# Performance work log

Measured on AMD Instinct MI355X. Metric: run time of the kernel, lower is better.

## Reference

```python
import jax, jax.numpy as jnp
import numpy as np


def _nn_mean_sqdist(source, target):
    # source: [N,3], target: [M,3]
    s_norm = jnp.sum(source ** 2, axis=1, keepdims=True)          # [N,1]
    t_norm = jnp.sum(target ** 2, axis=1, keepdims=True)          # [M,1]
    dist = s_norm + t_norm.T - 2.0 * (source @ target.T)          # [N,M] squared dists
    return jnp.min(dist, axis=1).mean()


def setup_inputs() -> dict:
    key = jax.random.key(0)
    k1, k2 = jax.random.split(key)
    pred_positions = jax.random.normal(k1, (16384, 3), dtype=jnp.float32)
    target_positions = jax.random.normal(k2, (16384, 3), dtype=jnp.float32)
    return {"pred_positions": pred_positions, "target_positions": target_positions}


def reference(pred_positions, target_positions):
    d_pt = _nn_mean_sqdist(pred_positions, target_positions)
    d_tp = _nn_mean_sqdist(target_positions, pred_positions)  # use_bidirectional=True
    return (d_pt + d_tp) / 2.0
```

## Files before the change

kernel.cpp:

```cpp
#include <hip/hip_runtime.h>

#define TPB 256

typedef __attribute__((ext_vector_type(8))) short bf16x8;
typedef __attribute__((ext_vector_type(16))) float f32x16;

__device__ inline unsigned short f2bf(float f) {
    unsigned u = __float_as_uint(f);
    return (unsigned short)((u + 0x7FFFu + ((u >> 16) & 1u)) >> 16);
}
__device__ inline float bf2f(unsigned short h) {
    return __uint_as_float((unsigned)h << 16);
}
__device__ inline uint4 pack8(unsigned short s0, unsigned short s1,
                              unsigned short s2, unsigned short s3,
                              unsigned short s4, unsigned short s5,
                              unsigned short s6, unsigned short s7) {
    uint4 v;
    v.x = (unsigned)s0 | ((unsigned)s1 << 16);
    v.y = (unsigned)s2 | ((unsigned)s3 << 16);
    v.z = (unsigned)s4 | ((unsigned)s5 << 16);
    v.w = (unsigned)s6 | ((unsigned)s7 << 16);
    return v;
}
__device__ inline bf16x8 as_frag(uint4 v) {
    union { uint4 u; bf16x8 f; } c; c.u = v; return c.f;
}

__global__ __launch_bounds__(TPB) void prep_kernel(
        const float* __restrict__ a, const float* __restrict__ b,
        uint4* __restrict__ pAa, uint4* __restrict__ pBa,
        uint4* __restrict__ pAb, uint4* __restrict__ pBb,
        float* __restrict__ norms, unsigned* __restrict__ pmins,
        float* __restrict__ acc, unsigned* __restrict__ cnt, int n) {
    int idx = blockIdx.x * TPB + threadIdx.x;
    if (idx < 2 * n) {
        int isB = idx >= n;
        int i = isB ? idx - n : idx;
        const float* s = isB ? b : a;
        float x = s[3 * i], y = s[3 * i + 1], z = s[3 * i + 2];
        float w = x * x + y * y + z * z;
        norms[idx] = w;
        float ax = -2.0f * x, ay = -2.0f * y, az = -2.0f * z;
        unsigned short ahx = f2bf(ax), ahy = f2bf(ay), ahz = f2bf(az);
        unsigned short alx = f2bf(ax - bf2f(ahx));
        unsigned short aly = f2bf(ay - bf2f(ahy));
        unsigned short alz = f2bf(az - bf2f(ahz));
        unsigned short thx = f2bf(x), thy = f2bf(y), thz = f2bf(z);
        unsigned short tlx = f2bf(x - bf2f(thx));
        unsigned short tly = f2bf(y - bf2f(thy));
        unsigned short tlz = f2bf(z - bf2f(thz));
        unsigned short wh = f2bf(w);  float r1 = w - bf2f(wh);
        unsigned short wm = f2bf(r1); float r2 = r1 - bf2f(wm);
        unsigned short wl = f2bf(r2);
        const unsigned short ONE = 0x3F80;
        uint4* Ad = (isB ? pAb : pAa) + (size_t)i * 2;
        uint4* Bd = (isB ? pBb : pBa) + (size_t)i * 2;
        Ad[0] = pack8(ahx, ahy, ahz, alx, aly, alz, ahx, ahy);
        Ad[1] = pack8(ahz, ONE, ONE, ONE, alx, aly, alz, 0);
        Bd[0] = pack8(thx, thy, thz, thx, thy, thz, tlx, tly);
        Bd[1] = pack8(tlz, wh, wm, wl, tlx, tly, tlz, 0);
        pmins[idx] = 0xFFFFFFFFu;
    }
    if (idx == 0) { acc[0] = 0.0f; cnt[0] = 0u; }
}

__global__ __launch_bounds__(TPB, 4) void minpass_kernel(
        const uint4* __restrict__ pAa, const uint4* __restrict__ pBa,
        const uint4* __restrict__ pAb, const uint4* __restrict__ pBb,
        const float* __restrict__ norms, unsigned* __restrict__ pmins, int n) {
    const int TS = 8;
    const int NRB = n / 256;
    const int TGT = n / TS;
    const int NIT = TGT / 64;

    int bid = blockIdx.x;
    int dir = bid / (NRB * TS);
    int rem = bid % (NRB * TS);
    int rbk = rem / TS;
    int ts  = rem % TS;

    const uint4* __restrict__ Ap = dir ? pAb : pAa;
    const uint4* __restrict__ Bp = dir ? pBa : pBb;

    const int tid = threadIdx.x;
    const int wid = tid >> 6, lane = tid & 63;
    const int lr = lane & 31, lh = lane >> 5;

    const int rowbase = rbk * 256 + wid * 64;
    bf16x8 a0 = as_frag(Ap[(size_t)(rowbase + lr) * 2 + lh]);
    bf16x8 a1 = as_frag(Ap[(size_t)(rowbase + 32 + lr) * 2 + lh]);

    float rm0[16], rm1[16];
#pragma unroll
    for (int i = 0; i < 16; ++i) { rm0[i] = __builtin_inff(); rm1[i] = __builtin_inff(); }
    f32x16 z = {};

    const uint4* __restrict__ bp = Bp + (size_t)(ts * TGT + lr) * 2 + lh;

#define PAIR_ITER(B0, B1) do {                                                  \
    bf16x8 b0 = as_frag(B0), b1 = as_frag(B1);                                  \
    f32x16 dX = __builtin_amdgcn_mfma_f32_32x32x16_bf16(a0, b0, z, 0, 0, 0);    \
    f32x16 dY = __builtin_amdgcn_mfma_f32_32x32x16_bf16(a0, b1, z, 0, 0, 0);    \
    _Pragma("unroll")                                                           \
    for (int i = 0; i < 16; ++i)                                                \
        rm0[i] = fminf(rm0[i], fminf(dX[i], dY[i]));             \
    dX = __builtin_amdgcn_mfma_f32_32x32x16_bf16(a1, b0, z, 0, 0, 0);           \
    dY = __builtin_amdgcn_mfma_f32_32x32x16_bf16(a1, b1, z, 0, 0, 0);           \
    _Pragma("unroll")                                                           \
    for (int i = 0; i < 16; ++i)                                                \
        rm1[i] = fminf(rm1[i], fminf(dX[i], dY[i]));                            \
} while (0)

    uint4 P0 = bp[0], P1 = bp[64], P2 = bp[128], P3 = bp[192];
    for (int j = 0; j + 4 <= NIT; j += 2) {
        PAIR_ITER(P0, P1);
        P0 = bp[(size_t)(2 * j + 4) * 64];
        P1 = bp[(size_t)(2 * j + 5) * 64];
        PAIR_ITER(P2, P3);
        P2 = bp[(size_t)(2 * j + 6) * 64];
        P3 = bp[(size_t)(2 * j + 7) * 64];
    }
    PAIR_ITER(P0, P1);
    PAIR_ITER(P2, P3);

#pragma unroll
    for (int k = 1; k < 32; k <<= 1) {
#pragma unroll
        for (int i = 0; i < 16; ++i) {
            rm0[i] = fminf(rm0[i], __shfl_xor(rm0[i], k, 64));
            rm1[i] = fminf(rm1[i], __shfl_xor(rm1[i], k, 64));
        }
    }
    if (lr == 0) {
        unsigned* pm = pmins + (size_t)dir * n;
        const float* nb = norms + (dir ? n : 0);
        int rb0 = rowbase + lh * 4;
#pragma unroll
        for (int i = 0; i < 16; ++i) {
            int r = (i & 3) + ((i >> 2) << 3);
            int r0 = rb0 + r, r1 = rb0 + 32 + r;
            atomicMin(&pm[r0], __float_as_uint(rm0[i] + nb[r0]));
            atomicMin(&pm[r1], __float_as_uint(rm1[i] + nb[r1]));
        }
    }
#undef PAIR_ITER
}

__global__ __launch_bounds__(TPB) void finalize_kernel(
        const uint4* __restrict__ pmins, float* __restrict__ acc,
        unsigned* __restrict__ cnt, float* __restrict__ out, int n, int nblocks) {
    int i = blockIdx.x * TPB + threadIdx.x;
    uint4 v = pmins[i];
    float sum = __uint_as_float(v.x) + __uint_as_float(v.y)
              + __uint_as_float(v.z) + __uint_as_float(v.w);
    for (int off = 32; off > 0; off >>= 1)
        sum += __shfl_down(sum, off, 64);
    __shared__ float wsum[TPB / 64];
    int lane = threadIdx.x & 63, wid = threadIdx.x >> 6;
    if (lane == 0) wsum[wid] = sum;
    __syncthreads();
    if (threadIdx.x == 0) {
        float t = 0.0f;
        for (int w = 0; w < TPB / 64; ++w) t += wsum[w];
        atomicAdd(acc, t);
        __threadfence();
        unsigned old = atomicAdd(cnt, 1u);
        if (old == (unsigned)(nblocks - 1)) {
            float a0 = atomicAdd(acc, 0.0f);
            out[0] = a0 / (float)(2 * n);
        }
    }
}

extern "C" void kernel_launch(void* const* d_in, const int* in_sizes, int n_in,
                              void* d_out, int out_size, void* d_ws, size_t ws_size,
                              hipStream_t stream) {
    const float* a = (const float*)d_in[0];
    const float* b = (const float*)d_in[1];
    int n = in_sizes[0] / 3;
    float* out = (float*)d_out;
    char* ws = (char*)d_ws;
    float* acc = (float*)ws;
    unsigned* cnt = (unsigned*)(ws + 8);
    float* norms = (float*)(ws + 256);
    char* packs = ws + 256 + (size_t)2 * n * 4;
    size_t psz = (size_t)n * 32;
    uint4* pAa = (uint4*)(packs);
    uint4* pBa = (uint4*)(packs + psz);
    uint4* pAb = (uint4*)(packs + 2 * psz);
    uint4* pBb = (uint4*)(packs + 3 * psz);
    unsigned* pmins = (unsigned*)(packs + 4 * psz);

    prep_kernel<<<(2 * n + TPB - 1) / TPB, TPB, 0, stream>>>(
        a, b, pAa, pBa, pAb, pBb, norms, pmins, acc, cnt, n);
    int mblocks = 2 * (n / 256) * 8;
    minpass_kernel<<<mblocks, TPB, 0, stream>>>(
        pAa, pBa, pAb, pBb, norms, pmins, n);
    int fblocks = (2 * n / 4) / TPB;
    finalize_kernel<<<fblocks, TPB, 0, stream>>>(
        (const uint4*)pmins, acc, cnt, out, n, fblocks);
}
```

Before: 97.86 us.

## Fold both squared norms into the MFMA and issue four MFMAs per pair

The source-point norm is now packed into the A fragment (wh,wm,wl against ONE in B), so the MFMA output is the full squared distance. This removes the norms buffer, its writes in prep and the per-row norm loads and adds in the atomicMin epilogue. The alpha-split low terms of the dot product are dropped from the second k-half, which changes which cross terms enter the sum and may slightly reduce precision. The four MFMAs per pair are now issued back to back before a merged min loop, with the launch-bounds occupancy hint lowered from 4 to 3 to give room for the extra live accumulators.

Result: slower. 100.1 us (+2.3%).

```diff
diff --git a/kernel.cpp b/kernel.cpp
--- a/kernel.cpp
+++ b/kernel.cpp
@@ -30,17 +30,17 @@
 __global__ __launch_bounds__(TPB) void prep_kernel(
         const float* __restrict__ a, const float* __restrict__ b,
         uint4* __restrict__ pAa, uint4* __restrict__ pBa,
-        uint4* __restrict__ pAb, uint4* __restrict__ pBb,
-        float* __restrict__ norms, unsigned* __restrict__ pmins,
+        uint4* __restrict__ pAt, uint4* __restrict__ pBt,
+        unsigned* __restrict__ pmins,
         float* __restrict__ acc, unsigned* __restrict__ cnt, int n) {
     int idx = blockIdx.x * TPB + threadIdx.x;
+    const unsigned short ONE = 0x3F80;
     if (idx < 2 * n) {
-        int isB = idx >= n;
-        int i = isB ? idx - n : idx;
-        const float* s = isB ? b : a;
+        int isT = idx >= n;
+        int i = isT ? idx - n : idx;
+        const float* s = isT ? b : a;
         float x = s[3 * i], y = s[3 * i + 1], z = s[3 * i + 2];
         float w = x * x + y * y + z * z;
-        norms[idx] = w;
         float ax = -2.0f * x, ay = -2.0f * y, az = -2.0f * z;
         unsigned short ahx = f2bf(ax), ahy = f2bf(ay), ahz = f2bf(az);
         unsigned short alx = f2bf(ax - bf2f(ahx));
@@ -53,26 +53,25 @@
         unsigned short wh = f2bf(w);  float r1 = w - bf2f(wh);
         unsigned short wm = f2bf(r1); float r2 = r1 - bf2f(wm);
         unsigned short wl = f2bf(r2);
-        const unsigned short ONE = 0x3F80;
-        uint4* Ad = (isB ? pAb : pAa) + (size_t)i * 2;
-        uint4* Bd = (isB ? pBb : pBa) + (size_t)i * 2;
+        uint4* Ad = (isT ? pAt : pAa) + (size_t)i * 2;
+        uint4* Bd = (isT ? pBt : pBa) + (size_t)i * 2;
         Ad[0] = pack8(ahx, ahy, ahz, alx, aly, alz, ahx, ahy);
-        Ad[1] = pack8(ahz, ONE, ONE, ONE, alx, aly, alz, 0);
+        Ad[1] = pack8(ahz, wh, wm, wl, ONE, ONE, ONE, 0);
         Bd[0] = pack8(thx, thy, thz, thx, thy, thz, tlx, tly);
-        Bd[1] = pack8(tlz, wh, wm, wl, tlx, tly, tlz, 0);
+        Bd[1] = pack8(tlz, ONE, ONE, ONE, wh, wm, wl, 0);
         pmins[idx] = 0xFFFFFFFFu;
     }
     if (idx == 0) { acc[0] = 0.0f; cnt[0] = 0u; }
 }
 
-__global__ __launch_bounds__(TPB, 4) void minpass_kernel(
+__global__ __launch_bounds__(TPB, 3) void minpass_kernel(
         const uint4* __restrict__ pAa, const uint4* __restrict__ pBa,
-        const uint4* __restrict__ pAb, const uint4* __restrict__ pBb,
-        const float* __restrict__ norms, unsigned* __restrict__ pmins, int n) {
+        const uint4* __restrict__ pAt, const uint4* __restrict__ pBt,
+        unsigned* __restrict__ pmins, int n) {
     const int TS = 8;
     const int NRB = n / 256;
     const int TGT = n / TS;
-    const int NIT = TGT / 64;
+    const int NP = TGT / 64;
 
     int bid = blockIdx.x;
     int dir = bid / (NRB * TS);
@@ -80,8 +79,8 @@
     int rbk = rem / TS;
     int ts  = rem % TS;
 
-    const uint4* __restrict__ Ap = dir ? pAb : pAa;
-    const uint4* __restrict__ Bp = dir ? pBa : pBb;
+    const uint4* __restrict__ Ap = dir ? pAt : pAa;
+    const uint4* __restrict__ Bp = dir ? pBa : pBt;
 
     const int tid = threadIdx.x;
     const int wid = tid >> 6, lane = tid & 63;
@@ -100,29 +99,29 @@
 
 #define PAIR_ITER(B0, B1) do {                                                  \
     bf16x8 b0 = as_frag(B0), b1 = as_frag(B1);                                  \
-    f32x16 dX = __builtin_amdgcn_mfma_f32_32x32x16_bf16(a0, b0, z, 0, 0, 0);    \
-    f32x16 dY = __builtin_amdgcn_mfma_f32_32x32x16_bf16(a0, b1, z, 0, 0, 0);    \
+    f32x16 d00 = __builtin_amdgcn_mfma_f32_32x32x16_bf16(a0, b0, z, 0, 0, 0);   \
+    f32x16 d01 = __builtin_amdgcn_mfma_f32_32x32x16_bf16(a0, b1, z, 0, 0, 0);   \
+    f32x16 d10 = __builtin_amdgcn_mfma_f32_32x32x16_bf16(a1, b0, z, 0, 0, 0);   \
+    f32x16 d11 = __builtin_amdgcn_mfma_f32_32x32x16_bf16(a1, b1, z, 0, 0, 0);   \
     _Pragma("unroll")                                                           \
-    for (int i = 0; i < 16; ++i)                                                \
-        rm0[i] = fminf(rm0[i], fminf(dX[i], dY[i]));             \
-    dX = __builtin_amdgcn_mfma_f32_32x32x16_bf16(a1, b0, z, 0, 0, 0);           \
-    dY = __builtin_amdgcn_mfma_f32_32x32x16_bf16(a1, b1, z, 0, 0, 0);           \
-    _Pragma("unroll")                                                           \
-    for (int i = 0; i < 16; ++i)                                                \
-        rm1[i] = fminf(rm1[i], fminf(dX[i], dY[i]));                            \
+    for (int i = 0; i < 16; ++i) {                                              \
+        rm0[i] = fminf(rm0[i], fminf(d00[i], d01[i]));           \
+        rm1[i] = fminf(rm1[i], fminf(d10[i], d11[i]));           \
+    }                                                                           \
 } while (0)
 
     uint4 P0 = bp[0], P1 = bp[64], P2 = bp[128], P3 = bp[192];
-    for (int j = 0; j + 4 <= NIT; j += 2) {
+    for (int p = 0; p + 4 <= NP; p += 2) {
         PAIR_ITER(P0, P1);
-        P0 = bp[(size_t)(2 * j + 4) * 64];
-        P1 = bp[(size_t)(2 * j + 5) * 64];
+        P0 = bp[(size_t)(2 * p + 4) * 64];
+        P1 = bp[(size_t)(2 * p + 5) * 64];
         PAIR_ITER(P2, P3);
-        P2 = bp[(size_t)(2 * j + 6) * 64];
-        P3 = bp[(size_t)(2 * j + 7) * 64];
+        P2 = bp[(size_t)(2 * p + 6) * 64];
+        P3 = bp[(size_t)(2 * p + 7) * 64];
     }
     PAIR_ITER(P0, P1);
     PAIR_ITER(P2, P3);
+#undef PAIR_ITER
 
 #pragma unroll
     for (int k = 1; k < 32; k <<= 1) {
@@ -134,17 +133,14 @@
     }
     if (lr == 0) {
         unsigned* pm = pmins + (size_t)dir * n;
-        const float* nb = norms + (dir ? n : 0);
         int rb0 = rowbase + lh * 4;
 #pragma unroll
         for (int i = 0; i < 16; ++i) {
             int r = (i & 3) + ((i >> 2) << 3);
-            int r0 = rb0 + r, r1 = rb0 + 32 + r;
-            atomicMin(&pm[r0], __float_as_uint(rm0[i] + nb[r0]));
-            atomicMin(&pm[r1], __float_as_uint(rm1[i] + nb[r1]));
+            atomicMin(&pm[rb0 + r], __float_as_uint(rm0[i]));
+            atomicMin(&pm[rb0 + 32 + r], __float_as_uint(rm1[i]));
         }
     }
-#undef PAIR_ITER
 }
 
 __global__ __launch_bounds__(TPB) void finalize_kernel(
@@ -183,20 +179,19 @@
     char* ws = (char*)d_ws;
     float* acc = (float*)ws;
     unsigned* cnt = (unsigned*)(ws + 8);
-    float* norms = (float*)(ws + 256);
-    char* packs = ws + 256 + (size_t)2 * n * 4;
+    char* packs = ws + 256;
     size_t psz = (size_t)n * 32;
     uint4* pAa = (uint4*)(packs);
     uint4* pBa = (uint4*)(packs + psz);
-    uint4* pAb = (uint4*)(packs + 2 * psz);
-    uint4* pBb = (uint4*)(packs + 3 * psz);
+    uint4* pAt = (uint4*)(packs + 2 * psz);
+    uint4* pBt = (uint4*)(packs + 3 * psz);
     unsigned* pmins = (unsigned*)(packs + 4 * psz);
 
     prep_kernel<<<(2 * n + TPB - 1) / TPB, TPB, 0, stream>>>(
-        a, b, pAa, pBa, pAb, pBb, norms, pmins, acc, cnt, n);
+        a, b, pAa, pBa, pAt, pBt, pmins, acc, cnt, n);
     int mblocks = 2 * (n / 256) * 8;
     minpass_kernel<<<mblocks, TPB, 0, stream>>>(
-        pAa, pBa, pAb, pBb, norms, pmins, n);
+        pAa, pBa, pAt, pBt, pmins, n);
     int fblocks = (2 * n / 4) / TPB;
     finalize_kernel<<<fblocks, TPB, 0, stream>>>(
         (const uint4*)pmins, acc, cnt, out, n, fblocks);
```
